# Kernel tuning notes

Measured on AMD Instinct MI355X. Metric: run time of the kernel, lower is better.

Reference implementation:

```python
import jax, jax.numpy as jnp
import numpy as np
from jax import lax

B, T, MEL, D, H, NC = 8, 256, 128, 192, 4, 20
C_EVENT, C_SCENE = 8, 64
ETA, LR, ALPHA = 0.9, 0.1, 0.01  # memory momentum, write lr, forget rate
EPS = 1e-5


def _ln(x, g, b):
    m = x.mean(-1, keepdims=True)
    v = ((x - m) ** 2).mean(-1, keepdims=True)
    return (x - m) / jnp.sqrt(v + EPS) * g + b


def _mem_step(x, t, M, S, Wk, Wv, Wq, chunk):
    # x: [B,D]; M,S: [B,D,D]. Titans-style neural memory, updated every `chunk` steps.
    k = x @ Wk
    v = x @ Wv
    q = x @ Wq
    err = v - jnp.einsum('bd,bde->be', k, M)          # surprise / prediction error
    S_new = ETA * S + LR * jnp.einsum('bd,be->bde', k, err)
    M_new = (1.0 - ALPHA) * M + S_new
    upd = (t % chunk) == 0
    S = jnp.where(upd, S_new, S)
    M = jnp.where(upd, M_new, M)
    out = jnp.einsum('bd,bde->be', q, M)              # retrieval
    return out, M, S


def setup_inputs() -> dict:
    key = jax.random.key(0)
    ks = jax.random.split(key, 24)
    w = lambda k, shp, s=0.05: jax.random.normal(k, shp, dtype=jnp.float32) * s
    inp = {
        'x': jax.random.normal(ks[0], (B, T, MEL), dtype=jnp.float32),
        'W_in': w(ks[1], (MEL, D)), 'b_in': jnp.zeros((D,), jnp.float32),
        # MHA at seq_len=1: softmax over one key -> weight 1, so only V and out proj matter
        'Wv_a': w(ks[2], (D, D)), 'bv_a': jnp.zeros((D,), jnp.float32),
        'Wo_a': w(ks[3], (D, D)), 'bo_a': jnp.zeros((D,), jnp.float32),
        # conformer conv module (degenerate seq_len=1: depthwise conv -> center tap)
        'ln1_g': jnp.ones((D,), jnp.float32), 'ln1_b': jnp.zeros((D,), jnp.float32),
        'pw1_w': w(ks[4], (D, 2 * D)), 'pw1_b': jnp.zeros((2 * D,), jnp.float32),
        'dw_w': w(ks[5], (D,), 0.2), 'dw_b': jnp.zeros((D,), jnp.float32),
        'bn_s': jnp.ones((D,), jnp.float32), 'bn_b': jnp.zeros((D,), jnp.float32),
        'pw2_w': w(ks[6], (D, D)), 'pw2_b': jnp.zeros((D,), jnp.float32),
        # theta (event) / delta (scene) neural memory projections
        'Wk_t': w(ks[7], (D, D)), 'Wv_t': w(ks[8], (D, D)), 'Wq_t': w(ks[9], (D, D)),
        'Wk_d': w(ks[10], (D, D)), 'Wv_d': w(ks[11], (D, D)), 'Wq_d': w(ks[12], (D, D)),
        'ln2_g': jnp.ones((D,), jnp.float32), 'ln2_b': jnp.zeros((D,), jnp.float32),
        'Wc': w(ks[13], (D, NC)), 'bc': jnp.zeros((NC,), jnp.float32),
    }
    return inp


def reference(x, W_in, b_in, Wv_a, bv_a, Wo_a, bo_a, ln1_g, ln1_b, pw1_w, pw1_b,
              dw_w, dw_b, bn_s, bn_b, pw2_w, pw2_b, Wk_t, Wv_t, Wq_t,
              Wk_d, Wv_d, Wq_d, ln2_g, ln2_b, Wc, bc):
    xp = x @ W_in + b_in                               # [B,T,D]

    def step(carry, inp):
        x_t, t = inp                                   # x_t: [B,D]
        Mt, St, Md, Sd = carry
        d_out, Md, Sd = _mem_step(x_t, t, Md, Sd, Wk_d, Wv_d, Wq_d, C_SCENE)
        x1 = x_t + 0.5 * d_out
        attn = (x1 @ Wv_a + bv_a) @ Wo_a + bo_a        # single-token self-attn
        x2 = x1 + attn
        h = _ln(x2, ln1_g, ln1_b)
        h = h @ pw1_w + pw1_b
        a, g = jnp.split(h, 2, axis=-1)
        h = a * jax.nn.sigmoid(g)                      # GLU
        h = h * dw_w + dw_b                            # depthwise conv center tap
        h = h * bn_s + bn_b                            # eval-mode BN
        h = jax.nn.silu(h)
        h = h @ pw2_w + pw2_b
        x3 = x2 + h
        t_out, Mt, St = _mem_step(x3, t, Mt, St, Wk_t, Wv_t, Wq_t, C_EVENT)
        x4 = x3 + 0.5 * t_out
        return (Mt, St, Md, Sd), _ln(x4, ln2_g, ln2_b)

    z = jnp.zeros((B, D, D), jnp.float32)
    xs = (jnp.swapaxes(xp, 0, 1), jnp.arange(T))       # [T,B,D], [T]
    _, ys = lax.scan(step, (z, z, z, z), xs)
    y = jnp.swapaxes(ys, 0, 1)                         # [B,T,D]
    pooled = y.mean(axis=1)
    return pooled @ Wc + bc                            # [B,NC]
```

## Files before the change

kernel.cpp:

```cpp
#include <hip/hip_runtime.h>
#include <math.h>

#define Bb 8
#define Tt 256
#define MEL 128
#define Dd 192
#define NCc 20
#define ND 4
#define NT 32
#define ETAc 0.9f
#define LRc 0.1f
#define MDEC 0.99f
#define EPSc 1e-5f
#define PT 4
#define PTILES 64
#define RTT 8
#define PADD 196

__device__ __forceinline__ float sigmoidf_(float x) {
    return 1.0f / (1.0f + __expf(-x));
}

__device__ __forceinline__ float memcoef(int n, int i) {
    float m = LRc, pw = LRc;
    for (int nn = i + 1; nn <= n; nn++) { pw *= ETAc; m = MDEC * m + pw; }
    return m;
}

__device__ __forceinline__ float dot4(float4 a, float4 b) {
    return a.x * b.x + a.y * b.y + a.z * b.z + a.w * b.w;
}

__global__ __launch_bounds__(192) void prep(
    const float* __restrict__ Wv_a, const float* __restrict__ Wo_a,
    const float* __restrict__ bv_a, const float* __restrict__ bo_a,
    const float* __restrict__ Wq_t, const float* __restrict__ Wq_d,
    const float* __restrict__ x, const float* __restrict__ W_in,
    const float* __restrict__ b_in, const float* __restrict__ Wk_d,
    const float* __restrict__ Wv_d,
    float* __restrict__ Wavo_ws, float* __restrict__ b_avo,
    float* __restrict__ WqtT, float* __restrict__ WqdT,
    float* __restrict__ Kd_ws, float* __restrict__ Vd_ws,
    float* __restrict__ pooled)
{
    __shared__ __align__(16) float smem[512];
    int blk = blockIdx.x, tid = threadIdx.x;

    if (blk < 192) {
        int m = blk;
        smem[tid] = Wv_a[m * Dd + tid];
        __syncthreads();
        int o = tid;
        float acc = 0.f;
        #pragma unroll 8
        for (int k = 0; k < Dd; k += 4) {
            acc += Wo_a[(k + 0) * Dd + o] * smem[k + 0];
            acc += Wo_a[(k + 1) * Dd + o] * smem[k + 1];
            acc += Wo_a[(k + 2) * Dd + o] * smem[k + 2];
            acc += Wo_a[(k + 3) * Dd + o] * smem[k + 3];
        }
        Wavo_ws[m * Dd + o] = acc;
        return;
    }
    if (blk == 192) {
        int o = tid;
        float s = bo_a[o];
        #pragma unroll 4
        for (int m = 0; m < Dd; m++) s += bv_a[m] * Wo_a[m * Dd + o];
        b_avo[o] = s;
        return;
    }
    if (blk < 241) {
        int r0 = 4 * (blk - 193);
        float4 v;
        v.x = Wq_t[(r0 + 0) * Dd + tid];
        v.y = Wq_t[(r0 + 1) * Dd + tid];
        v.z = Wq_t[(r0 + 2) * Dd + tid];
        v.w = Wq_t[(r0 + 3) * Dd + tid];
        *(float4*)&WqtT[tid * Dd + r0] = v;
        return;
    }
    if (blk < 289) {
        int r0 = 4 * (blk - 241);
        float4 v;
        v.x = Wq_d[(r0 + 0) * Dd + tid];
        v.y = Wq_d[(r0 + 1) * Dd + tid];
        v.z = Wq_d[(r0 + 2) * Dd + tid];
        v.w = Wq_d[(r0 + 3) * Dd + tid];
        *(float4*)&WqdT[tid * Dd + r0] = v;
        return;
    }
    if (blk == 321) {
        for (int q = tid; q < Bb * Dd; q += 192) pooled[q] = 0.f;
        return;
    }

    int q = blk - 289;
    int b = q >> 2, i = q & 3;
    float* XR = smem;
    float* XP = smem + 128;
    if (tid < 128) XR[tid] = x[((size_t)b * Tt + 64 * i) * MEL + tid];
    __syncthreads();
    {
        int o = tid;
        float acc = b_in[o];
        #pragma unroll 8
        for (int k = 0; k < MEL; k += 4) {
            acc += W_in[(k + 0) * Dd + o] * XR[k + 0];
            acc += W_in[(k + 1) * Dd + o] * XR[k + 1];
            acc += W_in[(k + 2) * Dd + o] * XR[k + 2];
            acc += W_in[(k + 3) * Dd + o] * XR[k + 3];
        }
        XP[o] = acc;
    }
    __syncthreads();
    {
        int o = tid;
        float ak = 0.f, av = 0.f;
        #pragma unroll 4
        for (int k = 0; k < Dd; k += 4) {
            float x0 = XP[k + 0], x1 = XP[k + 1], x2 = XP[k + 2], x3 = XP[k + 3];
            ak += Wk_d[(k + 0) * Dd + o] * x0 + Wk_d[(k + 1) * Dd + o] * x1
                + Wk_d[(k + 2) * Dd + o] * x2 + Wk_d[(k + 3) * Dd + o] * x3;
            av += Wv_d[(k + 0) * Dd + o] * x0 + Wv_d[(k + 1) * Dd + o] * x1
                + Wv_d[(k + 2) * Dd + o] * x2 + Wv_d[(k + 3) * Dd + o] * x3;
        }
        Kd_ws[(b * ND + i) * Dd + o] = ak;
        Vd_ws[(b * ND + i) * Dd + o] = av;
    }
}

__global__ __launch_bounds__(192) void delta_solve(
    const float* __restrict__ WqdT, const float* __restrict__ Kd_ws,
    float* __restrict__ Vd_ws, float* __restrict__ Ud_ws)
{
    int blk = blockIdx.x, b = blk / 5, role = blk % 5, tid = threadIdx.x;
    if (role == 0) {
        __shared__ __align__(16) float K4[ND][Dd], V4[ND][Dd];
        __shared__ float G[16], mc[16];
        for (int q = tid; q < ND * 48; q += 192) {
            int i = q / 48, c = q - i * 48;
            ((float4*)K4[i])[c] = ((const float4*)&Kd_ws[(b * ND + i) * Dd])[c];
            ((float4*)V4[i])[c] = ((const float4*)&Vd_ws[(b * ND + i) * Dd])[c];
        }
        __syncthreads();
        if (tid < 16) {
            int i = tid >> 2, j = tid & 3;
            float s = 0.f;
            for (int d = 0; d < Dd; d++) s += K4[i][d] * K4[j][d];
            G[tid] = s;
            mc[tid] = (j <= i) ? memcoef(i, j) : 0.f;
        }
        __syncthreads();
        for (int i = 1; i < ND; i++) {
            float acc = V4[i][tid];
            for (int m = 0; m < i; m++)
                acc -= mc[(i - 1) * ND + m] * G[i * ND + m] * V4[m][tid];
            V4[i][tid] = acc;
            __syncthreads();
        }
        for (int i = 0; i < ND; i++) Vd_ws[(b * ND + i) * Dd + tid] = V4[i][tid];
    } else {
        __shared__ float KS[Dd];
        int i = role - 1;
        KS[tid] = Kd_ws[(b * ND + i) * Dd + tid];
        __syncthreads();
        int o = tid;
        float acc = 0.f;
        #pragma unroll 8
        for (int k = 0; k < Dd; k += 4) {
            acc += WqdT[(k + 0) * Dd + o] * KS[k + 0];
            acc += WqdT[(k + 1) * Dd + o] * KS[k + 1];
            acc += WqdT[(k + 2) * Dd + o] * KS[k + 2];
            acc += WqdT[(k + 3) * Dd + o] * KS[k + 3];
        }
        Ud_ws[(b * ND + i) * Dd + o] = acc;
    }
}

__global__ __launch_bounds__(192) void pipeline(
    const float* __restrict__ x, const float* __restrict__ W_in,
    const float* __restrict__ b_in,
    const float* __restrict__ ln1_g, const float* __restrict__ ln1_b,
    const float* __restrict__ pw1_w, const float* __restrict__ pw1_b,
    const float* __restrict__ dw_w, const float* __restrict__ dw_b,
    const float* __restrict__ bn_s, const float* __restrict__ bn_b,
    const float* __restrict__ pw2_w, const float* __restrict__ pw2_b,
    const float* __restrict__ Wavo_ws, const float* __restrict__ b_avo,
    const float* __restrict__ Ed_ws, const float* __restrict__ Ud_ws,
    float* __restrict__ x3_ws)
{
    int blk = blockIdx.x;
    int b = blk >> 6, tile = blk & 63;
    int t0 = tile * PT, n = tile >> 4;
    int tid = threadIdx.x;

    __shared__ __align__(16) float XR[PT][MEL];
    __shared__ __align__(16) float XP[PT][Dd];
    __shared__ __align__(16) float ED[ND][PADD], UD[ND][PADD];
    __shared__ __align__(16) float X1[PT][Dd], X2[PT][Dd];
    __shared__ __align__(16) float LNX[PT][Dd], HG[PT][Dd];
    __shared__ float WQs[PT * ND];
    __shared__ float mv[PT][2];

    if (tid < 128) {
        int r = tid >> 5, c = tid & 31;
        ((float4*)XR[r])[c] = ((const float4*)&x[((size_t)b * Tt + t0 + r) * MEL])[c];
    }
    for (int q = tid; q < ND * 48 * 2; q += 192) {
        int which = q >= ND * 48;
        int qq = which ? q - ND * 48 : q;
        int i = qq / 48, c = qq - i * 48;
        if (!which) ((float4*)ED[i])[c] = ((const float4*)&Ed_ws[(b * ND + i) * Dd])[c];
        else        ((float4*)UD[i])[c] = ((const float4*)&Ud_ws[(b * ND + i) * Dd])[c];
    }
    __syncthreads();

    int o = tid;
    {
        float acc[PT];
        float bb = b_in[o];
        #pragma unroll
        for (int r = 0; r < PT; r++) acc[r] = bb;
        #pragma unroll 8
        for (int k = 0; k < MEL; k += 4) {
            float w0 = W_in[(k + 0) * Dd + o], w1 = W_in[(k + 1) * Dd + o];
            float w2 = W_in[(k + 2) * Dd + o], w3 = W_in[(k + 3) * Dd + o];
            #pragma unroll
            for (int r = 0; r < PT; r++) {
                float4 xv = *(const float4*)&XR[r][k];
                acc[r] += w0 * xv.x + w1 * xv.y + w2 * xv.z + w3 * xv.w;
            }
        }
        #pragma unroll
        for (int r = 0; r < PT; r++) XP[r][tid] = acc[r];
    }
    __syncthreads();

    if (tid < 128) {
        int r = tid >> 5, i = (tid >> 3) & 3, c = tid & 7;
        float s = 0.f;
        const float* xp = XP[r];
        const float* u = UD[i];
        #pragma unroll
        for (int j = 0; j < 24; j++) s += xp[c * 24 + j] * u[c * 24 + j];
        s += __shfl_down(s, 4, 8);
        s += __shfl_down(s, 2, 8);
        s += __shfl_down(s, 1, 8);
        if (c == 0) {
            float coef = (i <= n) ? memcoef(n, i) : 0.f;
            WQs[r * ND + i] = s * coef;
        }
    }
    __syncthreads();

    {
        #pragma unroll
        for (int r = 0; r < PT; r++) {
            float dout = WQs[r * ND + 0] * ED[0][tid] + WQs[r * ND + 1] * ED[1][tid]
                       + WQs[r * ND + 2] * ED[2][tid] + WQs[r * ND + 3] * ED[3][tid];
            X1[r][tid] = XP[r][tid] + 0.5f * dout;
        }
    }
    __syncthreads();

    {
        float acc[PT];
        float bb = b_avo[o];
        #pragma unroll
        for (int r = 0; r < PT; r++) acc[r] = bb;
        #pragma unroll 8
        for (int k = 0; k < Dd; k += 4) {
            float w0 = Wavo_ws[(k + 0) * Dd + o], w1 = Wavo_ws[(k + 1) * Dd + o];
            float w2 = Wavo_ws[(k + 2) * Dd + o], w3 = Wavo_ws[(k + 3) * Dd + o];
            #pragma unroll
            for (int r = 0; r < PT; r++) {
                float4 xv = *(const float4*)&X1[r][k];
                acc[r] += w0 * xv.x + w1 * xv.y + w2 * xv.z + w3 * xv.w;
            }
        }
        #pragma unroll
        for (int r = 0; r < PT; r++) X2[r][tid] = X1[r][tid] + acc[r];
    }
    __syncthreads();

    if (tid < 128) {
        int r = tid >> 5, j = tid & 31;
        float s = 0.f, sq = 0.f;
        for (int d = j; d < Dd; d += 32) { float v = X2[r][d]; s += v; sq += v * v; }
        for (int off = 16; off > 0; off >>= 1) {
            s += __shfl_down(s, off, 32); sq += __shfl_down(sq, off, 32);
        }
        if (j == 0) {
            float mean = s / Dd;
            mv[r][0] = mean;
            mv[r][1] = rsqrtf(sq / Dd - mean * mean + EPSc);
        }
    }
    __syncthreads();
    {
        float g = ln1_g[tid], bb = ln1_b[tid];
        #pragma unroll
        for (int r = 0; r < PT; r++)
            LNX[r][tid] = (X2[r][tid] - mv[r][0]) * mv[r][1] * g + bb;
    }
    __syncthreads();

    {
        float aa[PT], gg[PT];
        float ba = pw1_b[o], bg = pw1_b[o + Dd];
        #pragma unroll
        for (int r = 0; r < PT; r++) { aa[r] = ba; gg[r] = bg; }
        #pragma unroll 4
        for (int k = 0; k < Dd; k += 4) {
            float wa0 = pw1_w[(k + 0) * 2 * Dd + o], wg0 = pw1_w[(k + 0) * 2 * Dd + Dd + o];
            float wa1 = pw1_w[(k + 1) * 2 * Dd + o], wg1 = pw1_w[(k + 1) * 2 * Dd + Dd + o];
            float wa2 = pw1_w[(k + 2) * 2 * Dd + o], wg2 = pw1_w[(k + 2) * 2 * Dd + Dd + o];
            float wa3 = pw1_w[(k + 3) * 2 * Dd + o], wg3 = pw1_w[(k + 3) * 2 * Dd + Dd + o];
            #pragma unroll
            for (int r = 0; r < PT; r++) {
                float4 xv = *(const float4*)&LNX[r][k];
                aa[r] += wa0 * xv.x + wa1 * xv.y + wa2 * xv.z + wa3 * xv.w;
                gg[r] += wg0 * xv.x + wg1 * xv.y + wg2 * xv.z + wg3 * xv.w;
            }
        }
        float dww = dw_w[o], dwb = dw_b[o], bns = bn_s[o], bnb = bn_b[o];
        #pragma unroll
        for (int r = 0; r < PT; r++) {
            float h = aa[r] * sigmoidf_(gg[r]);
            h = h * dww + dwb;
            h = h * bns + bnb;
            h = h * sigmoidf_(h);
            HG[r][tid] = h;
        }
    }
    __syncthreads();

    {
        float acc[PT];
        float bb = pw2_b[o];
        #pragma unroll
        for (int r = 0; r < PT; r++) acc[r] = bb;
        #pragma unroll 8
        for (int k = 0; k < Dd; k += 4) {
            float w0 = pw2_w[(k + 0) * Dd + o], w1 = pw2_w[(k + 1) * Dd + o];
            float w2 = pw2_w[(k + 2) * Dd + o], w3 = pw2_w[(k + 3) * Dd + o];
            #pragma unroll
            for (int r = 0; r < PT; r++) {
                float4 xv = *(const float4*)&HG[r][k];
                acc[r] += w0 * xv.x + w1 * xv.y + w2 * xv.z + w3 * xv.w;
            }
        }
        #pragma unroll
        for (int r = 0; r < PT; r++)
            x3_ws[((size_t)b * Tt + t0 + r) * Dd + tid] = X2[r][tid] + acc[r];
    }
}

__global__ __launch_bounds__(192) void theta_projU(
    const float* __restrict__ x3_ws,
    const float* __restrict__ Wk_t, const float* __restrict__ Wv_t,
    const float* __restrict__ WqtT,
    float* __restrict__ Kt_ws, float* __restrict__ Vt_ws,
    float* __restrict__ Ut_ws)
{
    int blk = blockIdx.x, b = blk >> 5, i = blk & 31;
    int tid = threadIdx.x;
    __shared__ float XS[Dd];
    __shared__ float KS[Dd];

    XS[tid] = x3_ws[((size_t)b * Tt + 8 * i) * Dd + tid];
    __syncthreads();

    int o = tid;
    float ak = 0.f, av = 0.f;
    #pragma unroll 4
    for (int k = 0; k < Dd; k += 4) {
        float x0 = XS[k + 0], x1 = XS[k + 1], x2 = XS[k + 2], x3 = XS[k + 3];
        ak += Wk_t[(k + 0) * Dd + o] * x0 + Wk_t[(k + 1) * Dd + o] * x1
            + Wk_t[(k + 2) * Dd + o] * x2 + Wk_t[(k + 3) * Dd + o] * x3;
        av += Wv_t[(k + 0) * Dd + o] * x0 + Wv_t[(k + 1) * Dd + o] * x1
            + Wv_t[(k + 2) * Dd + o] * x2 + Wv_t[(k + 3) * Dd + o] * x3;
    }
    Kt_ws[(b * NT + i) * Dd + o] = ak;
    Vt_ws[(b * NT + i) * Dd + o] = av;
    KS[o] = ak;
    __syncthreads();

    float au = 0.f;
    #pragma unroll 8
    for (int k = 0; k < Dd; k += 4) {
        au += WqtT[(k + 0) * Dd + o] * KS[k + 0];
        au += WqtT[(k + 1) * Dd + o] * KS[k + 1];
        au += WqtT[(k + 2) * Dd + o] * KS[k + 2];
        au += WqtT[(k + 3) * Dd + o] * KS[k + 3];
    }
    Ut_ws[(b * NT + i) * Dd + o] = au;
}

__global__ __launch_bounds__(192) void theta_solve(
    const float* __restrict__ Kt_ws, float* __restrict__ Vt_ws)
{
    int b = blockIdx.x, tid = threadIdx.x;
    __shared__ __align__(16) float K[NT][PADD], E[NT][PADD];
    __shared__ float G[NT * NT], mc[NT * NT];

    for (int q = tid; q < NT * 48; q += 192) {
        int i = q / 48, c = q - i * 48;
        ((float4*)K[i])[c] = ((const float4*)&Kt_ws[(b * NT + i) * Dd])[c];
        ((float4*)E[i])[c] = ((const float4*)&Vt_ws[(b * NT + i) * Dd])[c];
    }
    if (tid < NT) {
        int i = tid;
        float m = 0.f, pw = LRc;
        for (int nn = 0; nn < NT; nn++) {
            float v;
            if (nn < i) v = 0.f;
            else if (nn == i) { m = LRc; v = m; }
            else { pw *= ETAc; m = MDEC * m + pw; v = m; }
            mc[nn * NT + i] = v;
        }
    }
    __syncthreads();
    for (int p = tid; p < NT * NT; p += 192) {
        int i = p >> 5, j = p & 31;
        const float4* ki = (const float4*)K[i];
        const float4* kj = (const float4*)K[j];
        float s = 0.f;
        #pragma unroll 4
        for (int kk = 0; kk < 48; kk++) s += dot4(ki[kk], kj[kk]);
        G[p] = s;
    }
    __syncthreads();
    for (int i = 1; i < NT; i++) {
        float acc = E[i][tid];
        #pragma unroll 4
        for (int m = 0; m < i; m++)
            acc -= mc[(i - 1) * NT + m] * G[i * NT + m] * E[m][tid];
        E[i][tid] = acc;
        __syncthreads();
    }
    for (int i = 0; i < NT; i++) Vt_ws[(b * NT + i) * Dd + tid] = E[i][tid];
}

__global__ __launch_bounds__(256) void retrieve(
    const float* __restrict__ x3_ws, const float* __restrict__ Ut_ws,
    const float* __restrict__ Et_ws, const float* __restrict__ ln2_g,
    const float* __restrict__ ln2_b, float* __restrict__ pooled)
{
    int blk = blockIdx.x, b = blk >> 5, tile = blk & 31;
    int t0 = tile * RTT, n = tile;
    int tid = threadIdx.x;

    __shared__ __align__(16) float UT[NT][PADD];
    __shared__ __align__(16) float XS[RTT][PADD];
    __shared__ float WQ[RTT * NT];
    __shared__ float mv[RTT][2];

    for (int q = tid; q < NT * 48; q += 256) {
        int i = q / 48, c = q - i * 48;
        ((float4*)UT[i])[c] = ((const float4*)&Ut_ws[(b * NT + i) * Dd])[c];
    }
    for (int q = tid; q < RTT * 48; q += 256) {
        int r = q / 48, c = q - r * 48;
        ((float4*)XS[r])[c] = ((const float4*)&x3_ws[((size_t)b * Tt + t0 + r) * Dd])[c];
    }
    __syncthreads();

    {
        int r = tid >> 5, i = tid & 31;
        const float4* u4 = (const float4*)UT[i];
        const float4* x4 = (const float4*)XS[r];
        float s = 0.f;
        #pragma unroll 8
        for (int kk = 0; kk < 48; kk++) s += dot4(u4[kk], x4[kk]);
        float coef = (i <= n) ? memcoef(n, i) : 0.f;
        WQ[tid] = s * coef;
    }
    __syncthreads();

    if (tid < Dd) {
        float acc[RTT] = {};
        #pragma unroll 4
        for (int i = 0; i < NT; i++) {
            float e = Et_ws[(b * NT + i) * Dd + tid];
            #pragma unroll
            for (int r = 0; r < RTT; r++) acc[r] += WQ[r * NT + i] * e;
        }
        #pragma unroll
        for (int r = 0; r < RTT; r++) XS[r][tid] += 0.5f * acc[r];
    }
    __syncthreads();

    {
        int r = tid >> 5, j = tid & 31;
        float s = 0.f, sq = 0.f;
        for (int d = j; d < Dd; d += 32) { float v = XS[r][d]; s += v; sq += v * v; }
        for (int off = 16; off > 0; off >>= 1) {
            s += __shfl_down(s, off, 32); sq += __shfl_down(sq, off, 32);
        }
        if (j == 0) {
            float mean = s / Dd;
            mv[r][0] = mean;
            mv[r][1] = rsqrtf(sq / Dd - mean * mean + EPSc);
        }
    }
    __syncthreads();

    if (tid < Dd) {
        float g = ln2_g[tid], bb = ln2_b[tid];
        float sum = 0.f;
        #pragma unroll
        for (int r = 0; r < RTT; r++)
            sum += (XS[r][tid] - mv[r][0]) * mv[r][1] * g + bb;
        atomicAdd(&pooled[b * Dd + tid], sum);
    }
}

__global__ __launch_bounds__(192) void head(
    const float* __restrict__ pooled, const float* __restrict__ Wc,
    const float* __restrict__ bc, float* __restrict__ out)
{
    int tid = threadIdx.x;
    if (tid < Bb * NCc) {
        int b = tid / NCc, c = tid - b * NCc;
        float s = 0.f;
        for (int d = 0; d < Dd; d++) s += pooled[b * Dd + d] * Wc[d * NCc + c];
        out[tid] = s * (1.0f / Tt) + bc[c];
    }
}

extern "C" void kernel_launch(void* const* d_in, const int* in_sizes, int n_in,
                              void* d_out, int out_size, void* d_ws, size_t ws_size,
                              hipStream_t stream) {
    const float* x     = (const float*)d_in[0];
    const float* W_in  = (const float*)d_in[1];
    const float* b_in  = (const float*)d_in[2];
    const float* Wv_a  = (const float*)d_in[3];
    const float* bv_a  = (const float*)d_in[4];
    const float* Wo_a  = (const float*)d_in[5];
    const float* bo_a  = (const float*)d_in[6];
    const float* ln1_g = (const float*)d_in[7];
    const float* ln1_b = (const float*)d_in[8];
    const float* pw1_w = (const float*)d_in[9];
    const float* pw1_b = (const float*)d_in[10];
    const float* dw_w  = (const float*)d_in[11];
    const float* dw_b  = (const float*)d_in[12];
    const float* bn_s  = (const float*)d_in[13];
    const float* bn_b  = (const float*)d_in[14];
    const float* pw2_w = (const float*)d_in[15];
    const float* pw2_b = (const float*)d_in[16];
    const float* Wk_t  = (const float*)d_in[17];
    const float* Wv_t  = (const float*)d_in[18];
    const float* Wq_t  = (const float*)d_in[19];
    const float* Wk_d  = (const float*)d_in[20];
    const float* Wv_d  = (const float*)d_in[21];
    const float* Wq_d  = (const float*)d_in[22];
    const float* ln2_g = (const float*)d_in[23];
    const float* ln2_b = (const float*)d_in[24];
    const float* Wc    = (const float*)d_in[25];
    const float* bc    = (const float*)d_in[26];

    float* ws = (float*)d_ws;
    size_t off = 0;
    float* x3_ws   = ws + off; off += (size_t)Bb * Tt * Dd;
    float* Kd_ws   = ws + off; off += Bb * ND * Dd;
    float* Vd_ws   = ws + off; off += Bb * ND * Dd;
    float* Ud_ws   = ws + off; off += Bb * ND * Dd;
    float* Kt_ws   = ws + off; off += Bb * NT * Dd;
    float* Vt_ws   = ws + off; off += Bb * NT * Dd;
    float* Ut_ws   = ws + off; off += Bb * NT * Dd;
    float* pooled  = ws + off; off += Bb * Dd;
    float* Wavo_ws = ws + off; off += Dd * Dd;
    float* WqtT    = ws + off; off += Dd * Dd;
    float* WqdT    = ws + off; off += Dd * Dd;
    float* b_avo   = ws + off; off += Dd;

    prep<<<322, 192, 0, stream>>>(
        Wv_a, Wo_a, bv_a, bo_a, Wq_t, Wq_d,
        x, W_in, b_in, Wk_d, Wv_d,
        Wavo_ws, b_avo, WqtT, WqdT, Kd_ws, Vd_ws, pooled);
    delta_solve<<<Bb * 5, 192, 0, stream>>>(WqdT, Kd_ws, Vd_ws, Ud_ws);
    pipeline<<<Bb * PTILES, 192, 0, stream>>>(
        x, W_in, b_in, ln1_g, ln1_b, pw1_w, pw1_b, dw_w, dw_b,
        bn_s, bn_b, pw2_w, pw2_b, Wavo_ws, b_avo, Vd_ws, Ud_ws, x3_ws);
    theta_projU<<<Bb * NT, 192, 0, stream>>>(
        x3_ws, Wk_t, Wv_t, WqtT, Kt_ws, Vt_ws, Ut_ws);
    theta_solve<<<Bb, 192, 0, stream>>>(Kt_ws, Vt_ws);
    retrieve<<<Bb * 32, 256, 0, stream>>>(
        x3_ws, Ut_ws, Vt_ws, ln2_g, ln2_b, pooled);
    head<<<1, 192, 0, stream>>>(pooled, Wc, bc, (float*)d_out);
}
```

Baseline: 207.6 us.

## Fuse theta projections into pipeline, head into retrieve, and invert theta solve

Even-tile blocks of the pipeline kernel now compute the theta K/V/U projections from their first x3 row, so the separate theta_projU launch goes away. The classifier head moves into retrieve: a global atomic counter picks the last block to finish, and that block computes the output. theta_solve replaces its sequential forward substitution, which needed a barrier per row, with an explicit triangular-inverse matrix that is then applied to V. A redundant barrier in delta_solve is also dropped. Together these cut kernel launches and serial synchronization. The cost is extra work in half the pipeline blocks and a last-block fence protocol that relies on correct memory ordering.

```diff
diff --git a/kernel.cpp b/kernel.cpp
--- a/kernel.cpp
+++ b/kernel.cpp
@@ -13,9 +13,9 @@
 #define MDEC 0.99f
 #define EPSc 1e-5f
 #define PT 4
-#define PTILES 64
 #define RTT 8
 #define PADD 196
+#define UPAD 193
 
 __device__ __forceinline__ float sigmoidf_(float x) {
     return 1.0f / (1.0f + __expf(-x));
@@ -31,7 +31,7 @@
     return a.x * b.x + a.y * b.y + a.z * b.z + a.w * b.w;
 }
 
-__global__ __launch_bounds__(192) void prep(
+__global__ __launch_bounds__(192) void setup(
     const float* __restrict__ Wv_a, const float* __restrict__ Wo_a,
     const float* __restrict__ bv_a, const float* __restrict__ bo_a,
     const float* __restrict__ Wq_t, const float* __restrict__ Wq_d,
@@ -41,7 +41,7 @@
     float* __restrict__ Wavo_ws, float* __restrict__ b_avo,
     float* __restrict__ WqtT, float* __restrict__ WqdT,
     float* __restrict__ Kd_ws, float* __restrict__ Vd_ws,
-    float* __restrict__ pooled)
+    float* __restrict__ pooled, unsigned int* __restrict__ ctr)
 {
     __shared__ __align__(16) float smem[512];
     int blk = blockIdx.x, tid = threadIdx.x;
@@ -90,12 +90,13 @@
         *(float4*)&WqdT[tid * Dd + r0] = v;
         return;
     }
-    if (blk == 321) {
+    if (blk == 289) {
         for (int q = tid; q < Bb * Dd; q += 192) pooled[q] = 0.f;
+        if (tid == 0) *ctr = 0u;
         return;
     }
 
-    int q = blk - 289;
+    int q = blk - 290;
     int b = q >> 2, i = q & 3;
     float* XR = smem;
     float* XP = smem + 128;
@@ -157,7 +158,6 @@
             for (int m = 0; m < i; m++)
                 acc -= mc[(i - 1) * ND + m] * G[i * ND + m] * V4[m][tid];
             V4[i][tid] = acc;
-            __syncthreads();
         }
         for (int i = 0; i < ND; i++) Vd_ws[(b * ND + i) * Dd + tid] = V4[i][tid];
     } else {
@@ -188,7 +188,10 @@
     const float* __restrict__ pw2_w, const float* __restrict__ pw2_b,
     const float* __restrict__ Wavo_ws, const float* __restrict__ b_avo,
     const float* __restrict__ Ed_ws, const float* __restrict__ Ud_ws,
-    float* __restrict__ x3_ws)
+    const float* __restrict__ Wk_t, const float* __restrict__ Wv_t,
+    const float* __restrict__ WqtT,
+    float* __restrict__ x3_ws, float* __restrict__ Kt_ws,
+    float* __restrict__ Vt_ws, float* __restrict__ Ut_ws)
 {
     int blk = blockIdx.x;
     int b = blk >> 6, tile = blk & 63;
@@ -200,6 +203,8 @@
     __shared__ __align__(16) float ED[ND][PADD], UD[ND][PADD];
     __shared__ __align__(16) float X1[PT][Dd], X2[PT][Dd];
     __shared__ __align__(16) float LNX[PT][Dd], HG[PT][Dd];
+    __shared__ float X3row[Dd];
+    __shared__ float KTs[Dd];
     __shared__ float WQs[PT * ND];
     __shared__ float mv[PT][2];
 
@@ -352,63 +357,59 @@
             }
         }
         #pragma unroll
-        for (int r = 0; r < PT; r++)
-            x3_ws[((size_t)b * Tt + t0 + r) * Dd + tid] = X2[r][tid] + acc[r];
-    }
-}
-
-__global__ __launch_bounds__(192) void theta_projU(
-    const float* __restrict__ x3_ws,
-    const float* __restrict__ Wk_t, const float* __restrict__ Wv_t,
-    const float* __restrict__ WqtT,
-    float* __restrict__ Kt_ws, float* __restrict__ Vt_ws,
-    float* __restrict__ Ut_ws)
-{
-    int blk = blockIdx.x, b = blk >> 5, i = blk & 31;
-    int tid = threadIdx.x;
-    __shared__ float XS[Dd];
-    __shared__ float KS[Dd];
-
-    XS[tid] = x3_ws[((size_t)b * Tt + 8 * i) * Dd + tid];
-    __syncthreads();
-
-    int o = tid;
-    float ak = 0.f, av = 0.f;
-    #pragma unroll 4
-    for (int k = 0; k < Dd; k += 4) {
-        float x0 = XS[k + 0], x1 = XS[k + 1], x2 = XS[k + 2], x3 = XS[k + 3];
-        ak += Wk_t[(k + 0) * Dd + o] * x0 + Wk_t[(k + 1) * Dd + o] * x1
-            + Wk_t[(k + 2) * Dd + o] * x2 + Wk_t[(k + 3) * Dd + o] * x3;
-        av += Wv_t[(k + 0) * Dd + o] * x0 + Wv_t[(k + 1) * Dd + o] * x1
-            + Wv_t[(k + 2) * Dd + o] * x2 + Wv_t[(k + 3) * Dd + o] * x3;
-    }
-    Kt_ws[(b * NT + i) * Dd + o] = ak;
-    Vt_ws[(b * NT + i) * Dd + o] = av;
-    KS[o] = ak;
-    __syncthreads();
-
-    float au = 0.f;
-    #pragma unroll 8
-    for (int k = 0; k < Dd; k += 4) {
-        au += WqtT[(k + 0) * Dd + o] * KS[k + 0];
-        au += WqtT[(k + 1) * Dd + o] * KS[k + 1];
-        au += WqtT[(k + 2) * Dd + o] * KS[k + 2];
-        au += WqtT[(k + 3) * Dd + o] * KS[k + 3];
-    }
-    Ut_ws[(b * NT + i) * Dd + o] = au;
+        for (int r = 0; r < PT; r++) {
+            float v = X2[r][tid] + acc[r];
+            if (r == 0) X3row[tid] = v;
+            x3_ws[((size_t)b * Tt + t0 + r) * Dd + tid] = v;
+        }
+    }
+
+    if ((tile & 1) == 0) {
+        int i8 = tile >> 1;
+        __syncthreads();
+        {
+            float ak = 0.f, av = 0.f;
+            #pragma unroll 4
+            for (int k = 0; k < Dd; k += 4) {
+                float x0 = X3row[k + 0], x1v = X3row[k + 1];
+                float x2v = X3row[k + 2], x3v = X3row[k + 3];
+                ak += Wk_t[(k + 0) * Dd + o] * x0 + Wk_t[(k + 1) * Dd + o] * x1v
+                    + Wk_t[(k + 2) * Dd + o] * x2v + Wk_t[(k + 3) * Dd + o] * x3v;
+                av += Wv_t[(k + 0) * Dd + o] * x0 + Wv_t[(k + 1) * Dd + o] * x1v
+                    + Wv_t[(k + 2) * Dd + o] * x2v + Wv_t[(k + 3) * Dd + o] * x3v;
+            }
+            Kt_ws[(b * NT + i8) * Dd + o] = ak;
+            Vt_ws[(b * NT + i8) * Dd + o] = av;
+            KTs[o] = ak;
+        }
+        __syncthreads();
+        {
+            float au = 0.f;
+            #pragma unroll 8
+            for (int k = 0; k < Dd; k += 4) {
+                au += WqtT[(k + 0) * Dd + o] * KTs[k + 0]
+                    + WqtT[(k + 1) * Dd + o] * KTs[k + 1]
+                    + WqtT[(k + 2) * Dd + o] * KTs[k + 2]
+                    + WqtT[(k + 3) * Dd + o] * KTs[k + 3];
+            }
+            Ut_ws[(b * NT + i8) * Dd + o] = au;
+        }
+    }
 }
 
 __global__ __launch_bounds__(192) void theta_solve(
-    const float* __restrict__ Kt_ws, float* __restrict__ Vt_ws)
+    const float* __restrict__ Kt_ws, const float* __restrict__ Vt_ws,
+    float* __restrict__ Et_ws)
 {
     int b = blockIdx.x, tid = threadIdx.x;
-    __shared__ __align__(16) float K[NT][PADD], E[NT][PADD];
-    __shared__ float G[NT * NT], mc[NT * NT];
+    __shared__ __align__(16) float K[NT][PADD], V[NT][PADD];
+    __shared__ float G[NT * NT], mcc[NT * NT];
+    __shared__ float T[NT * 33];
 
     for (int q = tid; q < NT * 48; q += 192) {
         int i = q / 48, c = q - i * 48;
         ((float4*)K[i])[c] = ((const float4*)&Kt_ws[(b * NT + i) * Dd])[c];
-        ((float4*)E[i])[c] = ((const float4*)&Vt_ws[(b * NT + i) * Dd])[c];
+        ((float4*)V[i])[c] = ((const float4*)&Vt_ws[(b * NT + i) * Dd])[c];
     }
     if (tid < NT) {
         int i = tid;
@@ -418,7 +419,7 @@
             if (nn < i) v = 0.f;
             else if (nn == i) { m = LRc; v = m; }
             else { pw *= ETAc; m = MDEC * m + pw; v = m; }
-            mc[nn * NT + i] = v;
+            mcc[nn * NT + i] = v;
         }
     }
     __syncthreads();
@@ -432,34 +433,51 @@
         G[p] = s;
     }
     __syncthreads();
-    for (int i = 1; i < NT; i++) {
-        float acc = E[i][tid];
-        #pragma unroll 4
-        for (int m = 0; m < i; m++)
-            acc -= mc[(i - 1) * NT + m] * G[i * NT + m] * E[m][tid];
-        E[i][tid] = acc;
-        __syncthreads();
-    }
-    for (int i = 0; i < NT; i++) Vt_ws[(b * NT + i) * Dd + tid] = E[i][tid];
+    for (int p = tid; p < NT * NT; p += 192) {
+        int i = p >> 5, m = p & 31;
+        G[p] = (m < i) ? mcc[(i - 1) * NT + m] * G[p] : 0.f;
+    }
+    __syncthreads();
+    if (tid < NT) {
+        int j = tid;
+        T[j * 33 + j] = 1.f;
+        for (int i = j + 1; i < NT; i++) {
+            float s = 0.f;
+            for (int m = j; m < i; m++) s += G[i * NT + m] * T[m * 33 + j];
+            T[i * 33 + j] = -s;
+        }
+    }
+    __syncthreads();
+    {
+        for (int i = 0; i < NT; i++) {
+            float s = 0.f;
+            for (int j = 0; j <= i; j++) s += T[i * 33 + j] * V[j][tid];
+            Et_ws[(b * NT + i) * Dd + tid] = s;
+        }
+    }
 }
 
 __global__ __launch_bounds__(256) void retrieve(
     const float* __restrict__ x3_ws, const float* __restrict__ Ut_ws,
     const float* __restrict__ Et_ws, const float* __restrict__ ln2_g,
-    const float* __restrict__ ln2_b, float* __restrict__ pooled)
+    const float* __restrict__ ln2_b, float* __restrict__ pooled,
+    const float* __restrict__ Wc, const float* __restrict__ bc,
+    float* __restrict__ out, unsigned int* __restrict__ ctr)
 {
     int blk = blockIdx.x, b = blk >> 5, tile = blk & 31;
     int t0 = tile * RTT, n = tile;
     int tid = threadIdx.x;
 
-    __shared__ __align__(16) float UT[NT][PADD];
+    __shared__ float UT[NT][UPAD];
     __shared__ __align__(16) float XS[RTT][PADD];
     __shared__ float WQ[RTT * NT];
     __shared__ float mv[RTT][2];
-
-    for (int q = tid; q < NT * 48; q += 256) {
-        int i = q / 48, c = q - i * 48;
-        ((float4*)UT[i])[c] = ((const float4*)&Ut_ws[(b * NT + i) * Dd])[c];
+    __shared__ float PLD[Bb * Dd];
+    __shared__ bool isLast;
+
+    for (int q = tid; q < NT * Dd; q += 256) {
+        int i = q / Dd, c = q - i * Dd;
+        UT[i][c] = Ut_ws[(size_t)b * NT * Dd + q];
     }
     for (int q = tid; q < RTT * 48; q += 256) {
         int r = q / 48, c = q - r * 48;
@@ -469,11 +487,11 @@
 
     {
         int r = tid >> 5, i = tid & 31;
-        const float4* u4 = (const float4*)UT[i];
-        const float4* x4 = (const float4*)XS[r];
+        const float* u = UT[i];
+        const float* xr = XS[r];
         float s = 0.f;
         #pragma unroll 8
-        for (int kk = 0; kk < 48; kk++) s += dot4(u4[kk], x4[kk]);
+        for (int kk = 0; kk < Dd; kk++) s += u[kk] * xr[kk];
         float coef = (i <= n) ? memcoef(n, i) : 0.f;
         WQ[tid] = s * coef;
     }
@@ -515,18 +533,24 @@
             sum += (XS[r][tid] - mv[r][0]) * mv[r][1] * g + bb;
         atomicAdd(&pooled[b * Dd + tid], sum);
     }
-}
-
-__global__ __launch_bounds__(192) void head(
-    const float* __restrict__ pooled, const float* __restrict__ Wc,
-    const float* __restrict__ bc, float* __restrict__ out)
-{
-    int tid = threadIdx.x;
-    if (tid < Bb * NCc) {
-        int b = tid / NCc, c = tid - b * NCc;
-        float s = 0.f;
-        for (int d = 0; d < Dd; d++) s += pooled[b * Dd + d] * Wc[d * NCc + c];
-        out[tid] = s * (1.0f / Tt) + bc[c];
+
+    __threadfence();
+    if (tid == 0) {
+        unsigned int old = atomicAdd(ctr, 1u);
+        isLast = (old == (unsigned)(Bb * 32 - 1));
+    }
+    __syncthreads();
+    if (isLast) {
+        __threadfence();
+        for (int q = tid; q < Bb * Dd; q += 256)
+            PLD[q] = *(volatile const float*)&pooled[q];
+        __syncthreads();
+        if (tid < Bb * NCc) {
+            int bo = tid / NCc, c = tid - bo * NCc;
+            float s = 0.f;
+            for (int d = 0; d < Dd; d++) s += PLD[bo * Dd + d] * Wc[d * NCc + c];
+            out[tid] = s * (1.0f / Tt) + bc[c];
+        }
     }
 }
 
@@ -569,25 +593,25 @@
     float* Ud_ws   = ws + off; off += Bb * ND * Dd;
     float* Kt_ws   = ws + off; off += Bb * NT * Dd;
     float* Vt_ws   = ws + off; off += Bb * NT * Dd;
+    float* Et_ws   = ws + off; off += Bb * NT * Dd;
     float* Ut_ws   = ws + off; off += Bb * NT * Dd;
     float* pooled  = ws + off; off += Bb * Dd;
     float* Wavo_ws = ws + off; off += Dd * Dd;
     float* WqtT    = ws + off; off += Dd * Dd;
     float* WqdT    = ws + off; off += Dd * Dd;
     float* b_avo   = ws + off; off += Dd;
-
-    prep<<<322, 192, 0, stream>>>(
+    unsigned int* ctr = (unsigned int*)(ws + off); off += 1;
+
+    setup<<<322, 192, 0, stream>>>(
         Wv_a, Wo_a, bv_a, bo_a, Wq_t, Wq_d,
         x, W_in, b_in, Wk_d, Wv_d,
-        Wavo_ws, b_avo, WqtT, WqdT, Kd_ws, Vd_ws, pooled);
+        Wavo_ws, b_avo, WqtT, WqdT, Kd_ws, Vd_ws, pooled, ctr);
     delta_solve<<<Bb * 5, 192, 0, stream>>>(WqdT, Kd_ws, Vd_ws, Ud_ws);
-    pipeline<<<Bb * PTILES, 192, 0, stream>>>(
+    pipeline<<<Bb * 64, 192, 0, stream>>>(
         x, W_in, b_in, ln1_g, ln1_b, pw1_w, pw1_b, dw_w, dw_b,
-        bn_s, bn_b, pw2_w, pw2_b, Wavo_ws, b_avo, Vd_ws, Ud_ws, x3_ws);
-    theta_projU<<<Bb * NT, 192, 0, stream>>>(
-        x3_ws, Wk_t, Wv_t, WqtT, Kt_ws, Vt_ws, Ut_ws);
-    theta_solve<<<Bb, 192, 0, stream>>>(Kt_ws, Vt_ws);
+        bn_s, bn_b, pw2_w, pw2_b, Wavo_ws, b_avo, Vd_ws, Ud_ws,
+        Wk_t, Wv_t, WqtT, x3_ws, Kt_ws, Vt_ws, Ut_ws);
+    theta_solve<<<Bb, 192, 0, stream>>>(Kt_ws, Vt_ws, Et_ws);
     retrieve<<<Bb * 32, 256, 0, stream>>>(
-        x3_ws, Ut_ws, Vt_ws, ln2_g, ln2_b, pooled);
-    head<<<1, 192, 0, stream>>>(pooled, Wc, bc, (float*)d_out);
-}
+        x3_ws, Ut_ws, Et_ws, ln2_g, ln2_b, pooled, Wc, bc, (float*)d_out, ctr);
+}
```

Measured after the change: 224.7 us. +8.2%, slower.
